# Performance work log

Hardware: AMD Instinct MI355X
Metric: run time of the kernel (lower is better)

## Reference

```python
import jax, jax.numpy as jnp
import numpy as np

V, E, H, C_TAGS, B, T = 32000, 256, 200, 20, 64, 512
LN_EPS = 1e-5


def setup_inputs() -> dict:
    key = jax.random.key(0)
    ks = jax.random.split(key, 12)
    s = 0.05
    return {
        "words": jax.random.randint(ks[0], (B, T), 0, V),
        "seq_len": jax.random.randint(ks[1], (B,), T // 2, T + 1),
        "target": jax.random.randint(ks[2], (B, T), 0, C_TAGS),
        "embed_table": jax.random.normal(ks[3], (V, E)) * s,
        "ln_gamma": jnp.ones((E,)),
        "ln_beta": jnp.zeros((E,)),
        "w_ih_f": jax.random.normal(ks[4], (4 * H, E)) * s,
        "w_hh_f": jax.random.normal(ks[5], (4 * H, H)) * s,
        "b_f": jnp.zeros((4 * H,)),  # b_ih + b_hh folded together
        "w_ih_b": jax.random.normal(ks[6], (4 * H, E)) * s,
        "w_hh_b": jax.random.normal(ks[7], (4 * H, H)) * s,
        "b_b": jnp.zeros((4 * H,)),
        "fc_w": jax.random.normal(ks[8], (C_TAGS, 2 * H)) * s,
        "fc_b": jnp.zeros((C_TAGS,)),
        "trans": jax.random.normal(ks[9], (C_TAGS, C_TAGS)) * s,
        "start_scores": jax.random.normal(ks[10], (C_TAGS,)) * s,
        "end_scores": jax.random.normal(ks[11], (C_TAGS,)) * s,
    }


def _lstm_dir(x, m, w_ih, w_hh, b, reverse):
    """x: [T,B,E] time-major, m: [T,B] float mask. Packed-sequence semantics:
    carry only updates on valid steps (matters for the reverse direction)."""
    Hn = w_hh.shape[1]
    gates_x = jnp.einsum('tbe,ge->tbg', x, w_ih) + b  # [T,B,4H], batched GEMM

    def step(carry, xs):
        h, c = carry
        gx, mt = xs
        g = gx + h @ w_hh.T
        i, f, gg, o = jnp.split(g, 4, axis=-1)  # torch gate order i,f,g,o
        c_new = jax.nn.sigmoid(f) * c + jax.nn.sigmoid(i) * jnp.tanh(gg)
        h_new = jax.nn.sigmoid(o) * jnp.tanh(c_new)
        mt = mt[:, None]
        h = mt * h_new + (1.0 - mt) * h
        c = mt * c_new + (1.0 - mt) * c
        return (h, c), h

    init = (jnp.zeros((x.shape[1], Hn), x.dtype), jnp.zeros((x.shape[1], Hn), x.dtype))
    _, hs = jax.lax.scan(step, init, (gates_x, m), reverse=reverse)
    return hs  # [T,B,H]


def _crf_nll(logits, mask, target, trans, start, end):
    """Linear-chain CRF NLL with start/end transitions. logits [B,T,C] (emissions),
    mask [B,T] float, target [B,T] int. Returns per-sample loss [B]."""
    # --- log partition via forward algorithm (scan over time) ---
    alpha0 = start[None, :] + logits[:, 0]  # [B,C]
    emits = jnp.swapaxes(logits, 0, 1)[1:]  # [T-1,B,C]
    ms = jnp.swapaxes(mask, 0, 1)[1:]       # [T-1,B]

    def step(alpha, xs):
        emit, mt = xs
        scores = alpha[:, :, None] + trans[None, :, :] + emit[:, None, :]  # [B,C,C]
        new = jax.nn.logsumexp(scores, axis=1)
        alpha = jnp.where(mt[:, None] > 0, new, alpha)
        return alpha, None

    alpha, _ = jax.lax.scan(step, alpha0, (emits, ms))
    logZ = jax.nn.logsumexp(alpha + end[None, :], axis=1)  # [B]

    # --- gold path score ---
    emit_gold = jnp.take_along_axis(logits, target[..., None], axis=2)[..., 0]  # [B,T]
    emit_score = jnp.sum(emit_gold * mask, axis=1)
    trans_gold = trans[target[:, :-1], target[:, 1:]]  # [B,T-1]
    trans_score = jnp.sum(trans_gold * mask[:, 1:], axis=1)
    last_idx = jnp.sum(mask, axis=1).astype(jnp.int32) - 1
    last_tag = jnp.take_along_axis(target, last_idx[:, None], axis=1)[:, 0]
    gold = emit_score + trans_score + start[target[:, 0]] + end[last_tag]
    return logZ - gold


def reference(words, seq_len, target, embed_table, ln_gamma, ln_beta,
              w_ih_f, w_hh_f, b_f, w_ih_b, w_hh_b, b_b,
              fc_w, fc_b, trans, start_scores, end_scores):
    # Embedding + LayerNorm
    x = embed_table[words]  # [B,T,E]
    mu = x.mean(-1, keepdims=True)
    var = ((x - mu) ** 2).mean(-1, keepdims=True)
    x = (x - mu) * jax.lax.rsqrt(var + LN_EPS) * ln_gamma + ln_beta

    mask = (jnp.arange(x.shape[1])[None, :] < seq_len[:, None]).astype(x.dtype)  # [B,T]
    xt = jnp.swapaxes(x, 0, 1)       # [T,B,E]
    mt = jnp.swapaxes(mask, 0, 1)    # [T,B]

    # BiLSTM (num_layers=1)
    hf = _lstm_dir(xt, mt, w_ih_f, w_hh_f, b_f, reverse=False)
    hb = _lstm_dir(xt, mt, w_ih_b, w_hh_b, b_b, reverse=True)
    feats = jnp.swapaxes(jnp.concatenate([hf, hb], axis=-1), 0, 1)  # [B,T,2H]

    # fc + dropout (eval: identity) + log_softmax emissions
    feats = feats @ fc_w.T + fc_b
    logits = jax.nn.log_softmax(feats, axis=-1)

    loss = _crf_nll(logits, mask, target, trans, start_scores, end_scores)
    return loss.mean()
```

## Files before the change

### kernel.cpp

```cpp
#include <hip/hip_runtime.h>

#define TT 512
#define BB 64
#define EE 256
#define HH 200
#define GG 800
#define CC 20
#define MM (BB * TT)

typedef _Float16 f16x8 __attribute__((ext_vector_type(8)));
typedef float    f32x4 __attribute__((ext_vector_type(4)));
typedef _Float16 f16x2 __attribute__((ext_vector_type(2)));
typedef int      i32x4 __attribute__((ext_vector_type(4)));

#if __has_builtin(__builtin_amdgcn_mfma_f32_16x16x32_f16)
#define HAVE_MFMA_F16 1
#else
#define HAVE_MFMA_F16 0
#endif

__device__ __forceinline__ float bf2f(unsigned short u) {
  return __uint_as_float(((unsigned int)u) << 16);
}
__device__ __forceinline__ unsigned short f2bf(float f) {
  unsigned int u = __float_as_uint(f);
  return (unsigned short)((u + 0x7fffu + ((u >> 16) & 1u)) >> 16);
}
__device__ __forceinline__ float sigf(float x) { return 1.0f / (1.0f + __expf(-x)); }
__device__ __forceinline__ float tanhfast(float x) {
  return 1.0f - 2.0f / (__expf(2.0f * x) + 1.0f);
}
__device__ __forceinline__ f16x2 bfpair_to_h2(unsigned int p) {
  f16x2 r;
  r[0] = (_Float16)bf2f((unsigned short)(p & 0xffffu));
  r[1] = (_Float16)bf2f((unsigned short)(p >> 16));
  return r;
}
__device__ __forceinline__ int h2i(f16x2 h) {
  union { f16x2 h; int i; } u; u.h = h; return u.i;
}
__device__ __forceinline__ f16x2 i2h2(int i) {
  union { int i; f16x2 h; } u; u.i = i; return u.h;
}
__device__ __forceinline__ float dot2acc(f16x2 a, f16x2 b, float c) {
#if __has_builtin(__builtin_amdgcn_fdot2)
  return __builtin_amdgcn_fdot2(a, b, c, false);
#else
  return c + (float)a[0] * (float)b[0] + (float)a[1] * (float)b[1];
#endif
}

#define NSEG 14
struct CvtArgs { const void* src[NSEG]; };
__constant__ const int cvt_cum[NSEG + 1] = {
    0, 8192000, 8192256, 8192512, 8397312, 8557312, 8558112,
    8762912, 8922912, 8923712, 8931712, 8931732, 8932132, 8932152, 8932172};

__global__ __launch_bounds__(256) void k_convert(CvtArgs a,
                                                 unsigned short* __restrict__ dst) {
  const bool f32mode = (((const unsigned int*)a.src[1])[0] == 0x3F800000u);
  int gi0 = (blockIdx.x * 256 + threadIdx.x) * 4;
#pragma unroll
  for (int r = 0; r < 4; ++r) {
    int gi = gi0 + r;
    if (gi >= cvt_cum[NSEG]) return;
    int seg = 0;
#pragma unroll
    for (int s = 1; s < NSEG; ++s) seg += (gi >= cvt_cum[s]) ? 1 : 0;
    int local = gi - cvt_cum[seg];
    unsigned short v;
    if (f32mode) v = f2bf(((const float*)a.src[seg])[local]);
    else         v = ((const unsigned short*)a.src[seg])[local];
    dst[gi] = v;
  }
}

__global__ __launch_bounds__(256) void k_embed_ln(
    const int* __restrict__ words, const unsigned short* __restrict__ etab,
    const unsigned short* __restrict__ gamma, const unsigned short* __restrict__ beta,
    unsigned short* __restrict__ x) {
  int m = blockIdx.x;
  int e = threadIdx.x;
  int w = words[m];
  float v = bf2f(etab[(size_t)w * EE + e]);
  float s = v, ss = v * v;
#pragma unroll
  for (int off = 32; off > 0; off >>= 1) {
    s += __shfl_xor(s, off, 64);
    ss += __shfl_xor(ss, off, 64);
  }
  __shared__ float red[2][4];
  int wv = e >> 6;
  if ((e & 63) == 0) { red[0][wv] = s; red[1][wv] = ss; }
  __syncthreads();
  float S = red[0][0] + red[0][1] + red[0][2] + red[0][3];
  float SS = red[1][0] + red[1][1] + red[1][2] + red[1][3];
  float mu = S * (1.0f / EE);
  float var = fmaxf(SS * (1.0f / EE) - mu * mu, 0.0f);
  float nrm = (v - mu) * rsqrtf(var + 1e-5f) * bf2f(gamma[e]) + bf2f(beta[e]);
  x[(size_t)m * EE + e] = f2bf(nrm);
}

#if HAVE_MFMA_F16
__global__ __launch_bounds__(256) void k_gates(
    const unsigned short* __restrict__ x,
    const unsigned short* __restrict__ wih_f, const unsigned short* __restrict__ wih_b,
    const unsigned short* __restrict__ bias_f, const unsigned short* __restrict__ bias_b,
    unsigned short* __restrict__ gates) {
  const int dir = blockIdx.z;
  const unsigned short* wih = dir ? wih_b : wih_f;
  const unsigned short* bias = dir ? bias_b : bias_f;
  const int m0 = blockIdx.x * 64;
  const int n0 = blockIdx.y * 64;
  __shared__ __align__(16) _Float16 As[64 * 32];
  __shared__ __align__(16) _Float16 Bs[64 * 32];
  const int tid = threadIdx.x;
  const int lane = tid & 63, wave = tid >> 6;
  const int wm = (wave >> 1) * 32, wn = (wave & 1) * 32;
  const int srow = tid >> 2, sq = tid & 3;
  const int mrow = lane & 15, q = lane >> 4;
  f32x4 acc[2][2] = {};
  for (int kk = 0; kk < EE; kk += 32) {
    union { int4 v; unsigned short u[8]; } ua, ub;
    ua.v = *(const int4*)(x + (size_t)(m0 + srow) * EE + kk + sq * 8);
    ub.v.x = 0; ub.v.y = 0; ub.v.z = 0; ub.v.w = 0;
    int n = n0 + srow;
    if (n < GG) ub.v = *(const int4*)(wih + (size_t)n * EE + kk + sq * 8);
    f16x8 af, bf;
#pragma unroll
    for (int r = 0; r < 8; ++r) {
      af[r] = (_Float16)bf2f(ua.u[r]);
      bf[r] = (_Float16)bf2f(ub.u[r]);
    }
    __syncthreads();
    *(f16x8*)(As + srow * 32 + sq * 8) = af;
    *(f16x8*)(Bs + srow * 32 + sq * 8) = bf;
    __syncthreads();
    f16x8 a0 = *(const f16x8*)(As + (wm + mrow) * 32 + q * 8);
    f16x8 a1 = *(const f16x8*)(As + (wm + 16 + mrow) * 32 + q * 8);
    f16x8 b0 = *(const f16x8*)(Bs + (wn + mrow) * 32 + q * 8);
    f16x8 b1 = *(const f16x8*)(Bs + (wn + 16 + mrow) * 32 + q * 8);
    acc[0][0] = __builtin_amdgcn_mfma_f32_16x16x32_f16(a0, b0, acc[0][0], 0, 0, 0);
    acc[0][1] = __builtin_amdgcn_mfma_f32_16x16x32_f16(a0, b1, acc[0][1], 0, 0, 0);
    acc[1][0] = __builtin_amdgcn_mfma_f32_16x16x32_f16(a1, b0, acc[1][0], 0, 0, 0);
    acc[1][1] = __builtin_amdgcn_mfma_f32_16x16x32_f16(a1, b1, acc[1][1], 0, 0, 0);
  }
#pragma unroll
  for (int im = 0; im < 2; ++im) {
#pragma unroll
    for (int in = 0; in < 2; ++in) {
      int n = n0 + wn + in * 16 + mrow;
      if (n < GG) {
        float bb = bf2f(bias[n]);
#pragma unroll
        for (int r = 0; r < 4; ++r) {
          int mg = m0 + wm + im * 16 + q * 4 + r;
          gates[((size_t)dir * MM + mg) * GG + n] = f2bf(acc[im][in][r] + bb);
        }
      }
    }
  }
}
#else
__global__ __launch_bounds__(256) void k_gates(
    const unsigned short* __restrict__ x,
    const unsigned short* __restrict__ wih_f, const unsigned short* __restrict__ wih_b,
    const unsigned short* __restrict__ bias_f, const unsigned short* __restrict__ bias_b,
    unsigned short* __restrict__ gates) {
  const int dir = blockIdx.z;
  const unsigned short* wih = dir ? wih_b : wih_f;
  const unsigned short* bias = dir ? bias_b : bias_f;
  const int m0 = blockIdx.x * 64;
  const int n0 = blockIdx.y * 64;
  for (int r = 0; r < 16; ++r) {
    int idx = threadIdx.x + 256 * r;
    int m = m0 + (idx >> 6), n = n0 + (idx & 63);
    if (n >= GG) continue;
    float acc = bf2f(bias[n]);
    const unsigned short* xr = x + (size_t)m * EE;
    const unsigned short* wr = wih + (size_t)n * EE;
    for (int k = 0; k < EE; ++k) acc += bf2f(xr[k]) * bf2f(wr[k]);
    gates[((size_t)dir * MM + m) * GG + n] = f2bf(acc);
  }
}
#endif

#define REP25(M) M(0) M(1) M(2) M(3) M(4) M(5) M(6) M(7) M(8) M(9) M(10) \
  M(11) M(12) M(13) M(14) M(15) M(16) M(17) M(18) M(19) M(20) M(21) M(22) \
  M(23) M(24)

__global__ __launch_bounds__(448) __attribute__((amdgpu_waves_per_eu(2, 2)))
void k_lstm(
    const unsigned short* __restrict__ gates,
    const unsigned short* __restrict__ whh_f, const unsigned short* __restrict__ whh_b,
    const int* __restrict__ seq_len,
    unsigned short* __restrict__ h_out) {
  const int b = blockIdx.x & (BB - 1);
  const int dir = blockIdx.x >> 6;
  const unsigned short* whh = dir ? whh_b : whh_f;
  const int tid = threadIdx.x;
  const int L = seq_len[b];
  __shared__ __align__(16) _Float16 hsh[2][HH + 8];
  const int e = tid >> 1;
  const int base = (tid & 1) * 200 + e;

#define DECLW(n) i32x4 wa##n = {0, 0, 0, 0}, wb##n = {0, 0, 0, 0};
  REP25(DECLW)
#undef DECLW

  if (tid < 400) {
    const unsigned short* wrA = whh + (size_t)base * HH;
    const unsigned short* wrB = whh + (size_t)(base + 400) * HH;
#define LOADW(n) { \
    int4 va = *(const int4*)(wrA + (n) * 8); \
    int4 vb = *(const int4*)(wrB + (n) * 8); \
    wa##n[0] = h2i(bfpair_to_h2((unsigned int)va.x)); \
    wa##n[1] = h2i(bfpair_to_h2((unsigned int)va.y)); \
    wa##n[2] = h2i(bfpair_to_h2((unsigned int)va.z)); \
    wa##n[3] = h2i(bfpair_to_h2((unsigned int)va.w)); \
    wb##n[0] = h2i(bfpair_to_h2((unsigned int)vb.x)); \
    wb##n[1] = h2i(bfpair_to_h2((unsigned int)vb.y)); \
    wb##n[2] = h2i(bfpair_to_h2((unsigned int)vb.z)); \
    wb##n[3] = h2i(bfpair_to_h2((unsigned int)vb.w)); }
    REP25(LOADW)
#undef LOADW
  }
#define PINW(n) asm("" : "+v"(wa##n), "+v"(wb##n));
  REP25(PINW)
#undef PINW

  if (tid < HH) { hsh[0][tid] = (_Float16)0.0f; hsh[1][tid] = (_Float16)0.0f; }
  float c_st = 0.0f, h_st = 0.0f;
  const unsigned short* g0 = gates + ((size_t)dir * MM + (size_t)b * TT) * GG;
  unsigned short* hobase = h_out + (size_t)(dir * BB + b) * TT * HH;
  float gxa = 0.0f, gxb = 0.0f;
  if (tid < 400) {
    int t0 = dir ? (L - 1) : 0;
    gxa = bf2f(g0[(size_t)t0 * GG + base]);
    gxb = bf2f(g0[(size_t)t0 * GG + base + 400]);
  }
  __syncthreads();
#pragma unroll 1
  for (int s = 0; s < L; ++s) {
    const int t = dir ? (L - 1 - s) : s;
    const int p = s & 1;
    float a0 = 0.0f, a1 = 0.0f;
    if (tid < 400) {
      int sn = (s + 1 < L) ? (s + 1) : s;
      int tn = dir ? (L - 1 - sn) : sn;
      float gna = bf2f(g0[(size_t)tn * GG + base]);
      float gnb = bf2f(g0[(size_t)tn * GG + base + 400]);
      float x0 = gxa, x1 = 0.0f, y0 = gxb, y1 = 0.0f;
      const _Float16* hp = hsh[p];
#define CHUNK(n) { \
      i32x4 hc = *(const i32x4*)(hp + (n) * 8); \
      x0 = dot2acc(i2h2(wa##n[0]), i2h2(hc[0]), x0); \
      x1 = dot2acc(i2h2(wa##n[1]), i2h2(hc[1]), x1); \
      x0 = dot2acc(i2h2(wa##n[2]), i2h2(hc[2]), x0); \
      x1 = dot2acc(i2h2(wa##n[3]), i2h2(hc[3]), x1); \
      y0 = dot2acc(i2h2(wb##n[0]), i2h2(hc[0]), y0); \
      y1 = dot2acc(i2h2(wb##n[1]), i2h2(hc[1]), y1); \
      y0 = dot2acc(i2h2(wb##n[2]), i2h2(hc[2]), y0); \
      y1 = dot2acc(i2h2(wb##n[3]), i2h2(hc[3]), y1); }
      REP25(CHUNK)
#undef CHUNK
      a0 = x0 + x1;
      a1 = y0 + y1;
      gxa = gna; gxb = gnb;
    }
    float n0 = __shfl_xor(a0, 1, 64);
    float n1 = __shfl_xor(a1, 1, 64);
    if (tid < 400 && !(tid & 1)) {
      float gi = a0, gg = a1, gf = n0, go = n1;
      float cn = sigf(gf) * c_st + sigf(gi) * tanhfast(gg);
      float hn = sigf(go) * tanhfast(cn);
      c_st = cn; h_st = hn;
      hsh[p ^ 1][e] = (_Float16)h_st;
      hobase[(size_t)t * HH + e] = f2bf(h_st);
    }
    __syncthreads();
  }
}
#undef REP25

__global__ __launch_bounds__(256) void k_fc(
    const unsigned short* __restrict__ h_out,
    const unsigned short* __restrict__ fc_w, const unsigned short* __restrict__ fc_b,
    float* __restrict__ logits) {
  __shared__ __align__(16) unsigned short hsh[4][2 * HH];
  const int wv = threadIdx.x >> 6, lane = threadIdx.x & 63;
  const int m = blockIdx.x * 4 + wv;
  if (lane < 25) {
    *(int4*)&hsh[wv][lane * 8] = *(const int4*)(h_out + (size_t)m * HH + lane * 8);
  } else if (lane < 50) {
    *(int4*)&hsh[wv][HH + (lane - 25) * 8] =
        *(const int4*)(h_out + (size_t)MM * HH + (size_t)m * HH + (lane - 25) * 8);
  }
  __syncthreads();
  float s = -3.0e38f;
  if (lane < CC) {
    s = bf2f(fc_b[lane]);
    const unsigned short* wrow = fc_w + lane * 2 * HH;
    for (int jj = 0; jj < 50; ++jj) {
      union { int4 v; unsigned short u[8]; } hw, ww;
      hw.v = *(const int4*)&hsh[wv][jj * 8];
      ww.v = *(const int4*)(wrow + jj * 8);
#pragma unroll
      for (int r = 0; r < 8; ++r) s += bf2f(hw.u[r]) * bf2f(ww.u[r]);
    }
  }
  float mx = s;
#pragma unroll
  for (int off = 32; off > 0; off >>= 1) mx = fmaxf(mx, __shfl_xor(mx, off, 64));
  float ex = (lane < CC) ? __expf(s - mx) : 0.0f;
  float sm = ex;
#pragma unroll
  for (int off = 32; off > 0; off >>= 1) sm += __shfl_xor(sm, off, 64);
  if (lane < CC) logits[(size_t)m * CC + lane] = s - mx - __logf(sm);
}

__global__ __launch_bounds__(64) void k_crf(
    const float* __restrict__ logits, const int* __restrict__ target,
    const int* __restrict__ seq_len, const unsigned short* __restrict__ trans,
    const unsigned short* __restrict__ startv, const unsigned short* __restrict__ endv,
    float* __restrict__ loss_b) {
  const int b = blockIdx.x, lane = threadIdx.x;
  const int L = seq_len[b];
  const int* tg = target + b * TT;
  const float* lg = logits + (size_t)b * TT * CC;
  float tcol[CC];
#pragma unroll
  for (int i = 0; i < CC; ++i) tcol[i] = (lane < CC) ? bf2f(trans[i * CC + lane]) : 0.0f;
  float g = 0.0f;
  for (int t = lane; t < TT; t += 64) {
    if (t < L) {
      g += lg[t * CC + tg[t]];
      if (t >= 1) g += bf2f(trans[tg[t - 1] * CC + tg[t]]);
    }
  }
#pragma unroll
  for (int off = 32; off > 0; off >>= 1) g += __shfl_xor(g, off, 64);
  float alpha = (lane < CC) ? (bf2f(startv[lane]) + lg[lane]) : -3.0e38f;
  for (int t = 1; t < L; ++t) {
    float e = (lane < CC) ? lg[t * CC + lane] : 0.0f;
    float sc[CC];
#pragma unroll
    for (int i = 0; i < CC; ++i) sc[i] = __shfl(alpha, i, 64) + tcol[i];
    float mx = sc[0];
#pragma unroll
    for (int i = 1; i < CC; ++i) mx = fmaxf(mx, sc[i]);
    float sm = 0.0f;
#pragma unroll
    for (int i = 0; i < CC; ++i) sm += __expf(sc[i] - mx);
    float na = mx + __logf(sm) + e;
    if (lane < CC) alpha = na;
  }
  float v = (lane < CC) ? (alpha + bf2f(endv[lane])) : -3.0e38f;
  float mx = v;
#pragma unroll
  for (int off = 32; off > 0; off >>= 1) mx = fmaxf(mx, __shfl_xor(mx, off, 64));
  float ex = (lane < CC) ? __expf(v - mx) : 0.0f;
#pragma unroll
  for (int off = 32; off > 0; off >>= 1) ex += __shfl_xor(ex, off, 64);
  if (lane == 0) {
    float logZ = mx + __logf(ex);
    float gold = g + bf2f(startv[tg[0]]) + bf2f(endv[tg[L - 1]]);
    loss_b[b] = logZ - gold;
  }
}

__global__ __launch_bounds__(64) void k_mean(const float* __restrict__ loss_b,
                                             unsigned int* __restrict__ out) {
  float v = loss_b[threadIdx.x];
#pragma unroll
  for (int off = 32; off > 0; off >>= 1) v += __shfl_xor(v, off, 64);
  if (threadIdx.x == 0) {
    float mean = v * (1.0f / BB);
    unsigned int lo = (unsigned int)f2bf(mean);
    unsigned int hi = __float_as_uint(mean) >> 16;
    out[0] = (hi << 16) | lo;
  }
}

extern "C" void kernel_launch(void* const* d_in, const int* in_sizes, int n_in,
                              void* d_out, int out_size, void* d_ws, size_t ws_size,
                              hipStream_t stream) {
  const int* words   = (const int*)d_in[0];
  const int* seq_len = (const int*)d_in[1];
  const int* target  = (const int*)d_in[2];

  char* ws = (char*)d_ws;
  const size_t x_off      = 0;
  const size_t gates_off  = x_off + 16777216;
  const size_t h_off      = gates_off + 104857600;
  const size_t logits_off = h_off + 26214400;
  const size_t loss_off   = logits_off + 2621440;
  const size_t cvt_off    = loss_off + 256;
  unsigned short* x      = (unsigned short*)(ws + x_off);
  unsigned short* gatesb = (unsigned short*)(ws + gates_off);
  unsigned short* h_out  = (unsigned short*)(ws + h_off);
  float* logits          = (float*)(ws + logits_off);
  float* loss_b          = (float*)(ws + loss_off);
  unsigned short* wcvt   = (unsigned short*)(ws + cvt_off);

  unsigned short* etab_c  = wcvt + 0;
  unsigned short* gamma_c = wcvt + 8192000;
  unsigned short* beta_c  = wcvt + 8192256;
  unsigned short* wih_f_c = wcvt + 8192512;
  unsigned short* whh_f_c = wcvt + 8397312;
  unsigned short* b_f_c   = wcvt + 8557312;
  unsigned short* wih_b_c = wcvt + 8558112;
  unsigned short* whh_b_c = wcvt + 8762912;
  unsigned short* b_b_c   = wcvt + 8922912;
  unsigned short* fc_w_c  = wcvt + 8923712;
  unsigned short* fc_b_c  = wcvt + 8931712;
  unsigned short* trans_c = wcvt + 8931732;
  unsigned short* start_c = wcvt + 8932132;
  unsigned short* end_c   = wcvt + 8932152;

  CvtArgs ca;
  for (int i = 0; i < NSEG; ++i) ca.src[i] = d_in[3 + i];
  const int total_cvt = 8932172;
  k_convert<<<(total_cvt + 1023) / 1024, 256, 0, stream>>>(ca, wcvt);

  k_embed_ln<<<MM, 256, 0, stream>>>(words, etab_c, gamma_c, beta_c, x);
  k_gates<<<dim3(MM / 64, 13, 2), 256, 0, stream>>>(x, wih_f_c, wih_b_c, b_f_c, b_b_c, gatesb);
  k_lstm<<<128, 448, 0, stream>>>(gatesb, whh_f_c, whh_b_c, seq_len, h_out);
  k_fc<<<MM / 4, 256, 0, stream>>>(h_out, fc_w_c, fc_b_c, logits);
  k_crf<<<BB, 64, 0, stream>>>(logits, target, seq_len, trans_c, start_c, end_c, loss_b);
  k_mean<<<1, 64, 0, stream>>>(loss_b, (unsigned int*)d_out);
}
```

Baseline: 1.166 ms.

## Repartition LSTM recurrence: one gate row per thread, spill rows to LDS and global

The recurrent kernel now uses 512 threads, each holding one W_hh row in registers instead of 400 threads each holding two rows. The remaining 288 rows are served from LDS (128 rows) and from global/L2 (160 rows) through an extra dot product. Gate pre-activations are exchanged through an LDS buffer with an added barrier per step, replacing the lane shuffle. An fp16 copy of W_hh is produced in the convert kernel and stored in the logits workspace region, which k_fc later overwrites. This trades fewer registers per thread and shorter per-thread dependency chains for an extra sync per step, uneven per-thread work, and global reads of weights on every step.

```diff
diff --git a/kernel.cpp b/kernel.cpp
--- a/kernel.cpp
+++ b/kernel.cpp
@@ -57,7 +57,8 @@
     8762912, 8922912, 8923712, 8931712, 8931732, 8932132, 8932152, 8932172};
 
 __global__ __launch_bounds__(256) void k_convert(CvtArgs a,
-                                                 unsigned short* __restrict__ dst) {
+                                                 unsigned short* __restrict__ dst,
+                                                 _Float16* __restrict__ whh16) {
   const bool f32mode = (((const unsigned int*)a.src[1])[0] == 0x3F800000u);
   int gi0 = (blockIdx.x * 256 + threadIdx.x) * 4;
 #pragma unroll
@@ -72,6 +73,8 @@
     if (f32mode) v = f2bf(((const float*)a.src[seg])[local]);
     else         v = ((const unsigned short*)a.src[seg])[local];
     dst[gi] = v;
+    if (seg == 4)      whh16[local]          = (_Float16)bf2f(v);
+    else if (seg == 7) whh16[160000 + local] = (_Float16)bf2f(v);
   }
 }
 
@@ -189,94 +192,81 @@
   M(11) M(12) M(13) M(14) M(15) M(16) M(17) M(18) M(19) M(20) M(21) M(22) \
   M(23) M(24)
 
-__global__ __launch_bounds__(448) __attribute__((amdgpu_waves_per_eu(2, 2)))
-void k_lstm(
+__global__ __launch_bounds__(512) void k_lstm(
     const unsigned short* __restrict__ gates,
-    const unsigned short* __restrict__ whh_f, const unsigned short* __restrict__ whh_b,
+    const _Float16* __restrict__ whh16,
     const int* __restrict__ seq_len,
     unsigned short* __restrict__ h_out) {
   const int b = blockIdx.x & (BB - 1);
   const int dir = blockIdx.x >> 6;
-  const unsigned short* whh = dir ? whh_b : whh_f;
+  const _Float16* W = whh16 + (size_t)dir * (GG * HH);
   const int tid = threadIdx.x;
   const int L = seq_len[b];
+  __shared__ __align__(16) _Float16 ldsw[128 * HH];
   __shared__ __align__(16) _Float16 hsh[2][HH + 8];
-  const int e = tid >> 1;
-  const int base = (tid & 1) * 200 + e;
-
-#define DECLW(n) i32x4 wa##n = {0, 0, 0, 0}, wb##n = {0, 0, 0, 0};
+  __shared__ float gbuf[GG];
+
+  const _Float16* wr = W + (size_t)tid * HH;
+#define DECLW(n) i32x4 w##n = *(const i32x4*)(wr + (n) * 8);
   REP25(DECLW)
 #undef DECLW
-
-  if (tid < 400) {
-    const unsigned short* wrA = whh + (size_t)base * HH;
-    const unsigned short* wrB = whh + (size_t)(base + 400) * HH;
-#define LOADW(n) { \
-    int4 va = *(const int4*)(wrA + (n) * 8); \
-    int4 vb = *(const int4*)(wrB + (n) * 8); \
-    wa##n[0] = h2i(bfpair_to_h2((unsigned int)va.x)); \
-    wa##n[1] = h2i(bfpair_to_h2((unsigned int)va.y)); \
-    wa##n[2] = h2i(bfpair_to_h2((unsigned int)va.z)); \
-    wa##n[3] = h2i(bfpair_to_h2((unsigned int)va.w)); \
-    wb##n[0] = h2i(bfpair_to_h2((unsigned int)vb.x)); \
-    wb##n[1] = h2i(bfpair_to_h2((unsigned int)vb.y)); \
-    wb##n[2] = h2i(bfpair_to_h2((unsigned int)vb.z)); \
-    wb##n[3] = h2i(bfpair_to_h2((unsigned int)vb.w)); }
-    REP25(LOADW)
-#undef LOADW
-  }
-#define PINW(n) asm("" : "+v"(wa##n), "+v"(wb##n));
+#define PINW(n) asm("" : "+v"(w##n));
   REP25(PINW)
 #undef PINW
 
+  for (int idx = tid; idx < 128 * 25; idx += 512) {
+    int r = idx / 25, c = idx - r * 25;
+    *(i32x4*)(ldsw + r * HH + c * 8) =
+        *(const i32x4*)(W + (size_t)(512 + r) * HH + c * 8);
+  }
+  const bool hasX = tid < 288;
+  const int xrow = hasX ? (512 + tid) : 512;
+  const _Float16* xp = (tid < 128) ? (const _Float16*)(ldsw + tid * HH)
+                                   : (W + (size_t)xrow * HH);
   if (tid < HH) { hsh[0][tid] = (_Float16)0.0f; hsh[1][tid] = (_Float16)0.0f; }
   float c_st = 0.0f, h_st = 0.0f;
   const unsigned short* g0 = gates + ((size_t)dir * MM + (size_t)b * TT) * GG;
   unsigned short* hobase = h_out + (size_t)(dir * BB + b) * TT * HH;
-  float gxa = 0.0f, gxb = 0.0f;
-  if (tid < 400) {
-    int t0 = dir ? (L - 1) : 0;
-    gxa = bf2f(g0[(size_t)t0 * GG + base]);
-    gxb = bf2f(g0[(size_t)t0 * GG + base + 400]);
-  }
+  const int t0 = dir ? (L - 1) : 0;
+  float gxO = bf2f(g0[(size_t)t0 * GG + tid]);
+  float gxX = hasX ? bf2f(g0[(size_t)t0 * GG + 512 + tid]) : 0.0f;
   __syncthreads();
 #pragma unroll 1
   for (int s = 0; s < L; ++s) {
     const int t = dir ? (L - 1 - s) : s;
     const int p = s & 1;
-    float a0 = 0.0f, a1 = 0.0f;
-    if (tid < 400) {
-      int sn = (s + 1 < L) ? (s + 1) : s;
-      int tn = dir ? (L - 1 - sn) : sn;
-      float gna = bf2f(g0[(size_t)tn * GG + base]);
-      float gnb = bf2f(g0[(size_t)tn * GG + base + 400]);
-      float x0 = gxa, x1 = 0.0f, y0 = gxb, y1 = 0.0f;
-      const _Float16* hp = hsh[p];
+    int sn = (s + 1 < L) ? (s + 1) : s;
+    int tn = dir ? (L - 1 - sn) : sn;
+    float gnO = bf2f(g0[(size_t)tn * GG + tid]);
+    float gnX = hasX ? bf2f(g0[(size_t)tn * GG + 512 + tid]) : 0.0f;
+    float a0 = gxO, a1 = 0.0f, e0 = gxX, e1 = 0.0f;
+    const _Float16* hp = hsh[p];
 #define CHUNK(n) { \
-      i32x4 hc = *(const i32x4*)(hp + (n) * 8); \
-      x0 = dot2acc(i2h2(wa##n[0]), i2h2(hc[0]), x0); \
-      x1 = dot2acc(i2h2(wa##n[1]), i2h2(hc[1]), x1); \
-      x0 = dot2acc(i2h2(wa##n[2]), i2h2(hc[2]), x0); \
-      x1 = dot2acc(i2h2(wa##n[3]), i2h2(hc[3]), x1); \
-      y0 = dot2acc(i2h2(wb##n[0]), i2h2(hc[0]), y0); \
-      y1 = dot2acc(i2h2(wb##n[1]), i2h2(hc[1]), y1); \
-      y0 = dot2acc(i2h2(wb##n[2]), i2h2(hc[2]), y0); \
-      y1 = dot2acc(i2h2(wb##n[3]), i2h2(hc[3]), y1); }
-      REP25(CHUNK)
+    i32x4 hc = *(const i32x4*)(hp + (n) * 8); \
+    a0 = dot2acc(i2h2(w##n[0]), i2h2(hc[0]), a0); \
+    a1 = dot2acc(i2h2(w##n[1]), i2h2(hc[1]), a1); \
+    a0 = dot2acc(i2h2(w##n[2]), i2h2(hc[2]), a0); \
+    a1 = dot2acc(i2h2(w##n[3]), i2h2(hc[3]), a1); \
+    if (hasX) { \
+      i32x4 xw = *(const i32x4*)(xp + (n) * 8); \
+      e0 = dot2acc(i2h2(xw[0]), i2h2(hc[0]), e0); \
+      e1 = dot2acc(i2h2(xw[1]), i2h2(hc[1]), e1); \
+      e0 = dot2acc(i2h2(xw[2]), i2h2(hc[2]), e0); \
+      e1 = dot2acc(i2h2(xw[3]), i2h2(hc[3]), e1); } }
+    REP25(CHUNK)
 #undef CHUNK
-      a0 = x0 + x1;
-      a1 = y0 + y1;
-      gxa = gna; gxb = gnb;
-    }
-    float n0 = __shfl_xor(a0, 1, 64);
-    float n1 = __shfl_xor(a1, 1, 64);
-    if (tid < 400 && !(tid & 1)) {
-      float gi = a0, gg = a1, gf = n0, go = n1;
+    gbuf[tid] = a0 + a1;
+    if (hasX) gbuf[512 + tid] = e0 + e1;
+    gxO = gnO; gxX = gnX;
+    __syncthreads();
+    if (tid < HH) {
+      float gi = gbuf[tid], gf = gbuf[HH + tid];
+      float gg = gbuf[2 * HH + tid], go = gbuf[3 * HH + tid];
       float cn = sigf(gf) * c_st + sigf(gi) * tanhfast(gg);
       float hn = sigf(go) * tanhfast(cn);
       c_st = cn; h_st = hn;
-      hsh[p ^ 1][e] = (_Float16)h_st;
-      hobase[(size_t)t * HH + e] = f2bf(h_st);
+      hsh[p ^ 1][tid] = (_Float16)h_st;
+      hobase[(size_t)t * HH + tid] = f2bf(h_st);
     }
     __syncthreads();
   }
@@ -402,15 +392,14 @@
   float* logits          = (float*)(ws + logits_off);
   float* loss_b          = (float*)(ws + loss_off);
   unsigned short* wcvt   = (unsigned short*)(ws + cvt_off);
+  _Float16* whh16 = (_Float16*)(ws + logits_off);
 
   unsigned short* etab_c  = wcvt + 0;
   unsigned short* gamma_c = wcvt + 8192000;
   unsigned short* beta_c  = wcvt + 8192256;
   unsigned short* wih_f_c = wcvt + 8192512;
-  unsigned short* whh_f_c = wcvt + 8397312;
   unsigned short* b_f_c   = wcvt + 8557312;
   unsigned short* wih_b_c = wcvt + 8558112;
-  unsigned short* whh_b_c = wcvt + 8762912;
   unsigned short* b_b_c   = wcvt + 8922912;
   unsigned short* fc_w_c  = wcvt + 8923712;
   unsigned short* fc_b_c  = wcvt + 8931712;
@@ -421,11 +410,11 @@
   CvtArgs ca;
   for (int i = 0; i < NSEG; ++i) ca.src[i] = d_in[3 + i];
   const int total_cvt = 8932172;
-  k_convert<<<(total_cvt + 1023) / 1024, 256, 0, stream>>>(ca, wcvt);
+  k_convert<<<(total_cvt + 1023) / 1024, 256, 0, stream>>>(ca, wcvt, whh16);
 
   k_embed_ln<<<MM, 256, 0, stream>>>(words, etab_c, gamma_c, beta_c, x);
   k_gates<<<dim3(MM / 64, 13, 2), 256, 0, stream>>>(x, wih_f_c, wih_b_c, b_f_c, b_b_c, gatesb);
-  k_lstm<<<128, 448, 0, stream>>>(gatesb, whh_f_c, whh_b_c, seq_len, h_out);
+  k_lstm<<<128, 512, 0, stream>>>(gatesb, whh16, seq_len, h_out);
   k_fc<<<MM / 4, 256, 0, stream>>>(h_out, fc_w_c, fc_b_c, logits);
   k_crf<<<BB, 64, 0, stream>>>(logits, target, seq_len, trans_c, start_c, end_c, loss_b);
   k_mean<<<1, 64, 0, stream>>>(loss_b, (unsigned int*)d_out);
```

After: 2.505 ms. 2.15x slower.
